# Performance work log

Hardware: AMD Instinct MI355X
Metric: run time of the kernel (lower is better)

Reference implementation:

```python
import jax, jax.numpy as jnp
import numpy as np

N = 4096
IN_F = 256
F = 64      # out_features
H = 4       # heads
NEG_SLOPE = 0.2


def setup_inputs() -> dict:
    key = jax.random.key(0)
    k1, k2, k3, k4 = jax.random.split(key, 4)
    x = jax.random.normal(k1, (N, IN_F), dtype=jnp.float32)
    # symmetric random binary adjacency with self-loops (avoids empty softmax rows)
    adj = jax.random.bernoulli(k2, 0.5, (N, N)).astype(jnp.float32)
    adj = jnp.clip(adj + adj.T, 0.0, 1.0)
    adj = jnp.maximum(adj, jnp.eye(N, dtype=jnp.float32))
    W = jax.random.normal(k3, (IN_F, F * H), dtype=jnp.float32) * (1.0 / np.sqrt(IN_F))
    a = jax.random.normal(k4, (2 * F, 1), dtype=jnp.float32) * 0.1
    return {"x": x, "adj": adj, "W": W, "a": a}


def reference(x, adj, W, a):
    # h: [N, H, F]
    h = (x @ W).reshape(N, H, F)
    # e[i, j, h] = leakyrelu(a_l . h[i, h] + a_r . h[j, h])  -- avoids the O(N^2*H*2F) concat
    a_l = a[:F, 0]
    a_r = a[F:, 0]
    el = jnp.einsum('nhf,f->nh', h, a_l)  # [N, H]
    er = jnp.einsum('nhf,f->nh', h, a_r)  # [N, H]
    e = jax.nn.leaky_relu(el[:, None, :] + er[None, :, :], NEG_SLOPE)  # [N, N, H]
    e = jnp.where(adj[:, :, None] == 0, -jnp.inf, e)
    attention = jax.nn.softmax(e, axis=1)  # softmax over neighbors j
    h_prime = jnp.einsum('ijh,jhf->ihf', attention, h)  # [N, H, F]
    return h_prime.mean(axis=1)  # [N, F]  (heads > 1 -> mean over heads)
```

## Files before the change

### kernel.cpp

```cpp
#include <hip/hip_runtime.h>
#include <hip/hip_bf16.h>

#define NN 4096
#define LOG2E 1.44269504088896340736f

typedef __attribute__((ext_vector_type(8))) short s8v;
typedef __attribute__((ext_vector_type(4))) float f4v;

__device__ __forceinline__ unsigned fu(float x){ union{float f;unsigned u;}z; z.f=x; return z.u; }
__device__ __forceinline__ unsigned short f2bf_rne(float x){
  unsigned u = fu(x);
  u += 0x7fffu + ((u >> 16) & 1u);
  return (unsigned short)(u >> 16);
}
__device__ __forceinline__ unsigned pack2_rne(float a, float b){
  return (unsigned)f2bf_rne(a) | ((unsigned)f2bf_rne(b) << 16);
}

__global__ __launch_bounds__(256) void k1_proj(
    const float* __restrict__ x, const float* __restrict__ W,
    const float* __restrict__ a, unsigned short* __restrict__ Vf,
    float* __restrict__ el4, float* __restrict__ Qr, float* __restrict__ Sr)
{
  __shared__ float4 xs[512];
  const int t = threadIdx.x;
  const int r0 = blockIdx.x * 8;
  const float4* xg = (const float4*)(x + (size_t)r0 * 256);
  xs[t] = xg[t];
  xs[t + 256] = xg[t + 256];
  __syncthreads();

  float acc[8] = {0.f,0.f,0.f,0.f,0.f,0.f,0.f,0.f};
  const float* Wp = W + t;
  float w0 = Wp[0], w1 = Wp[256], w2 = Wp[512], w3 = Wp[768];
  #pragma unroll 1
  for (int k4 = 0; k4 < 64; ++k4) {
    const int kn = (k4 + 1) & 63;
    float nw0 = Wp[kn*1024 +   0];
    float nw1 = Wp[kn*1024 + 256];
    float nw2 = Wp[kn*1024 + 512];
    float nw3 = Wp[kn*1024 + 768];
    #pragma unroll
    for (int r = 0; r < 8; ++r) {
      float4 xv = xs[r*64 + k4];
      acc[r] = fmaf(xv.x, w0, acc[r]);
      acc[r] = fmaf(xv.y, w1, acc[r]);
      acc[r] = fmaf(xv.z, w2, acc[r]);
      acc[r] = fmaf(xv.w, w3, acc[r]);
    }
    w0 = nw0; w1 = nw1; w2 = nw2; w3 = nw3;
  }

  union { unsigned u[4]; s8v v; } pk;
  #pragma unroll
  for (int p = 0; p < 4; ++p)
    pk.u[p] = pack2_rne(acc[2*p], acc[2*p+1]);
  {
    const int hh = t >> 6, nf = (t >> 4) & 3, mm = t & 15;
    const int jblk = r0 >> 5, qq = (r0 >> 3) & 3;
    const size_t chunk = (size_t)(((hh * 128 + jblk) * 4 + nf) * 64 + qq * 16 + mm);
    *(s8v*)(Vf + chunk * 8) = pk.v;
  }

  const int f = t & 63, h = t >> 6;
  const float al = a[f], ar = a[64 + f];
  #pragma unroll
  for (int r = 0; r < 8; ++r) {
    float v = acc[r] * al;
    float u = acc[r] * ar;
    #pragma unroll
    for (int off = 32; off > 0; off >>= 1) {
      v += __shfl_xor(v, off);
      u += __shfl_xor(u, off);
    }
    if (f == 0) {
      el4[(r0 + r) * 4 + h] = v * LOG2E;
      float up = u * LOG2E;
      Qr[h * NN + (r0 + r)] = __builtin_amdgcn_exp2f(up);
      Sr[h * NN + (r0 + r)] = __builtin_amdgcn_exp2f(0.2f * up);
    }
  }
}

__global__ __launch_bounds__(256, 8) void k0_pack(
    const float* __restrict__ adj, const float* __restrict__ el4,
    const float* __restrict__ Qr, const float* __restrict__ Sr,
    unsigned long long* __restrict__ adjB, float* __restrict__ lsum)
{
  __shared__ float qsh[2048];
  const int t = threadIdx.x;
  const int w = t >> 6, l = t & 63;
  const int p = blockIdx.y;
  const int row = blockIdx.x * 4 + w;
  const int jwin = p * 256;

  {
    const int h = t >> 6;
    float4 qv = *(const float4*)(Qr + h * NN + jwin + l * 4);
    float4 sv = *(const float4*)(Sr + h * NN + jwin + l * 4);
    *(float4*)(qsh + h * 256 + l * 4) = qv;
    *(float4*)(qsh + 1024 + h * 256 + l * 4) = sv;
  }

  const float4 av = *(const float4*)(adj + (size_t)row * NN + jwin + l * 4);

  unsigned long long b0 = __ballot(av.x != 0.0f);
  unsigned long long b1 = __ballot(av.y != 0.0f);
  unsigned long long b2 = __ballot(av.z != 0.0f);
  unsigned long long b3 = __ballot(av.w != 0.0f);
  if (l == 0) {
    unsigned long long* dst = adjB + (size_t)row * 64 + p * 4;
    dst[0] = b0; dst[1] = b1; dst[2] = b2; dst[3] = b3;
  }

  float4 elv = *(const float4*)(el4 + row * 4);
  const float P[4] = { __builtin_amdgcn_exp2f(elv.x), __builtin_amdgcn_exp2f(elv.y),
                       __builtin_amdgcn_exp2f(elv.z), __builtin_amdgcn_exp2f(elv.w) };
  const float R[4] = { __builtin_amdgcn_exp2f(0.2f*elv.x), __builtin_amdgcn_exp2f(0.2f*elv.y),
                       __builtin_amdgcn_exp2f(0.2f*elv.z), __builtin_amdgcn_exp2f(0.2f*elv.w) };

  __syncthreads();

  float ls[4];
  #pragma unroll
  for (int h = 0; h < 4; ++h) {
    float4 qv = *(const float4*)(qsh + h * 256 + l * 4);
    float4 sv = *(const float4*)(qsh + 1024 + h * 256 + l * 4);
    float s;
    s  = av.x * fmaxf(P[h] * qv.x, R[h] * sv.x);
    s  = fmaf(av.y, fmaxf(P[h] * qv.y, R[h] * sv.y), s);
    s  = fmaf(av.z, fmaxf(P[h] * qv.z, R[h] * sv.z), s);
    s  = fmaf(av.w, fmaxf(P[h] * qv.w, R[h] * sv.w), s);
    ls[h] = s;
  }
  #pragma unroll
  for (int h = 0; h < 4; ++h) {
    float v = ls[h];
    #pragma unroll
    for (int off = 32; off > 0; off >>= 1) v += __shfl_xor(v, off);
    ls[h] = v;
  }
  if (l == 0) {
    #pragma unroll
    for (int h = 0; h < 4; ++h)
      atomicAdd(&lsum[row * 4 + h], ls[h]);
  }
}

__global__ __launch_bounds__(256, 4) void k2_attn(
    const unsigned long long* __restrict__ adjB, const unsigned short* __restrict__ Vf,
    const float* __restrict__ el4, const float* __restrict__ lsum,
    const float* __restrict__ Qr, const float* __restrict__ Sr,
    float* __restrict__ out)
{
  __shared__ float qs[8192];
  const int t = threadIdx.x;
  const int w = t >> 6, l = t & 63;
  const int m = l & 15, q = l >> 4;
  const int i0 = blockIdx.x * 16;
  const int sw = blockIdx.y * 4 + w;
  const int i = i0 + m;
  const int jwin = sw * 256;

  {
    const int jc = l >> 3, qq = (l >> 1) & 3, hp = (l & 1) * 4;
    #pragma unroll
    for (int h = 0; h < 4; ++h) {
      float4 qv = *(const float4*)(Qr + h * NN + jwin + l * 4);
      float4 sv = *(const float4*)(Sr + h * NN + jwin + l * 4);
      float* cell = qs + (((w * 4 + h) * 8 + jc) * 4 + qq) * 16;
      *(float4*)(cell + hp) = qv;
      *(float4*)(cell + 8 + hp) = sv;
    }
  }

  float4 elv = *(const float4*)(el4 + i * 4);
  float4 ls4 = *(const float4*)(lsum + i * 4);
  float Pl[4], Rl[4];
  {
    const float el_[4] = {elv.x, elv.y, elv.z, elv.w};
    const float lv_[4] = {ls4.x, ls4.y, ls4.z, ls4.w};
    #pragma unroll
    for (int h = 0; h < 4; ++h) {
      const float inv = 1.0f / lv_[h];
      Pl[h] = __builtin_amdgcn_exp2f(el_[h]) * inv;
      Rl[h] = __builtin_amdgcn_exp2f(0.2f * el_[h]) * inv;
    }
  }

  const unsigned long long* bp = adjB + (size_t)i * 64 + sw * 4;
  unsigned long long b0 = bp[0], b1 = bp[1], b2 = bp[2], b3 = bp[3];

  f4v acc[4];
  #pragma unroll
  for (int nf = 0; nf < 4; ++nf) acc[nf] = (f4v){0.f, 0.f, 0.f, 0.f};

  const s8v* vfp = (const s8v*)Vf;
  s8v Bc[4];
  #pragma unroll
  for (int nf = 0; nf < 4; ++nf)
    Bc[nf] = vfp[(size_t)((0 * 128 + sw * 8 + 0) * 4 + nf) * 64 + l];

  #pragma unroll 1
  for (int jc = 0; jc < 8; ++jc) {
    const unsigned sh = jc * 8 + q * 2;
    const unsigned t0 = (unsigned)(b0 >> sh) & 3u;
    const unsigned t1 = (unsigned)(b1 >> sh) & 3u;
    const unsigned t2 = (unsigned)(b2 >> sh) & 3u;
    const unsigned t3 = (unsigned)(b3 >> sh) & 3u;
    float bitf[8];
    bitf[0] = (float)(t0 & 1u); bitf[4] = (float)(t0 >> 1);
    bitf[1] = (float)(t1 & 1u); bitf[5] = (float)(t1 >> 1);
    bitf[2] = (float)(t2 & 1u); bitf[6] = (float)(t2 >> 1);
    bitf[3] = (float)(t3 & 1u); bitf[7] = (float)(t3 >> 1);

    #pragma unroll
    for (int h = 0; h < 4; ++h) {
      const int hn = (h < 3) ? h + 1 : 0;
      const int jcn = (h < 3) ? jc : jc + 1;
      s8v Bn[4];
      #pragma unroll
      for (int nf = 0; nf < 4; ++nf)
        Bn[nf] = vfp[(size_t)((hn * 128 + sw * 8 + jcn) * 4 + nf) * 64 + l];

      const float* cell = qs + (((w * 4 + h) * 8 + jc) * 4 + q) * 16;
      float4 q0  = *(const float4*)(cell);
      float4 q1  = *(const float4*)(cell + 4);
      float4 sv0 = *(const float4*)(cell + 8);
      float4 sv1 = *(const float4*)(cell + 12);
      const float Ph = Pl[h], Rh = Rl[h];
      float s0 = bitf[0] * fmaxf(Ph * q0.x, Rh * sv0.x);
      float s1 = bitf[1] * fmaxf(Ph * q0.y, Rh * sv0.y);
      float s2 = bitf[2] * fmaxf(Ph * q0.z, Rh * sv0.z);
      float s3 = bitf[3] * fmaxf(Ph * q0.w, Rh * sv0.w);
      float s4 = bitf[4] * fmaxf(Ph * q1.x, Rh * sv1.x);
      float s5 = bitf[5] * fmaxf(Ph * q1.y, Rh * sv1.y);
      float s6 = bitf[6] * fmaxf(Ph * q1.z, Rh * sv1.z);
      float s7 = bitf[7] * fmaxf(Ph * q1.w, Rh * sv1.w);
      union { unsigned u[4]; s8v v; } A;
      A.u[0] = pack2_rne(s0, s1);
      A.u[1] = pack2_rne(s2, s3);
      A.u[2] = pack2_rne(s4, s5);
      A.u[3] = pack2_rne(s6, s7);
      #pragma unroll
      for (int nf = 0; nf < 4; ++nf)
        acc[nf] = __builtin_amdgcn_mfma_f32_16x16x32_bf16(A.v, Bc[nf], acc[nf], 0, 0, 0);
      #pragma unroll
      for (int nf = 0; nf < 4; ++nf) Bc[nf] = Bn[nf];
    }
  }

  __syncthreads();
  if (w > 0) {
    float* dst = qs + ((w - 1) * 64 + l) * 20;
    #pragma unroll
    for (int nf = 0; nf < 4; ++nf)
      *(f4v*)(dst + nf * 4) = acc[nf];
  }
  __syncthreads();
  if (w == 0) {
    const float* src = qs + l * 20;
    #pragma unroll
    for (int nf = 0; nf < 4; ++nf) {
      f4v s = acc[nf];
      s += *(const f4v*)(src +    0 + nf * 4);
      s += *(const f4v*)(src + 1280 + nf * 4);
      s += *(const f4v*)(src + 2560 + nf * 4);
      #pragma unroll
      for (int r = 0; r < 4; ++r) {
        int row = i0 + q * 4 + r;
        int col = nf * 16 + m;
        atomicAdd(&out[row * 64 + col], 0.25f * s[r]);
      }
    }
  }
}

extern "C" void kernel_launch(void* const* d_in, const int* in_sizes, int n_in,
                              void* d_out, int out_size, void* d_ws, size_t ws_size,
                              hipStream_t stream) {
  const float* x   = (const float*)d_in[0];
  const float* adj = (const float*)d_in[1];
  const float* W   = (const float*)d_in[2];
  const float* a   = (const float*)d_in[3];
  float* out = (float*)d_out;

  char* ws = (char*)d_ws;
  unsigned short* Vf = (unsigned short*)ws;
  float* el4 = (float*)(ws + (2u << 20));
  float* Qr  = (float*)(ws + (2u << 20) + (64u << 10));
  float* Sr  = (float*)(ws + (2u << 20) + (128u << 10));
  float* lsum= (float*)(ws + (2u << 20) + (192u << 10));
  unsigned long long* adjB = (unsigned long long*)(ws + (2u << 20) + (256u << 10));

  hipMemsetAsync(out, 0, (size_t)out_size * sizeof(float), stream);
  hipMemsetAsync(lsum, 0, NN * 4 * sizeof(float), stream);
  k1_proj<<<512, 256, 0, stream>>>(x, W, a, Vf, el4, Qr, Sr);
  k0_pack<<<dim3(1024, 16), 256, 0, stream>>>(adj, el4, Qr, Sr, adjB, lsum);
  k2_attn<<<dim3(256, 4), 256, 0, stream>>>(adjB, Vf, el4, lsum, Qr, Sr, out);
}
```

Measured before the change: 170.0 us.

## Coarsen adjacency pack kernel, replace lsum atomics with partial sums, deepen W prefetch

k0_pack now handles 1024 columns per block instead of 256. It issues four adjacency float4 loads up front and stages four windows of Q/S into shared memory. The per-row softmax denominators are written as four non-atomic partial sums, which k2_attn adds together. This removes the lsum memset and the atomic traffic. k1_proj also prefetches W two iterations ahead, at the cost of more registers and a larger shared array in k0 (32KB), which lowers occupancy.

Result: faster. 159.6 us (-6.1%).

```diff
diff --git a/kernel.cpp b/kernel.cpp
--- a/kernel.cpp
+++ b/kernel.cpp
@@ -32,10 +32,11 @@
 
   float acc[8] = {0.f,0.f,0.f,0.f,0.f,0.f,0.f,0.f};
   const float* Wp = W + t;
-  float w0 = Wp[0], w1 = Wp[256], w2 = Wp[512], w3 = Wp[768];
+  float wa0 = Wp[0],    wa1 = Wp[256],  wa2 = Wp[512],  wa3 = Wp[768];
+  float wb0 = Wp[1024], wb1 = Wp[1280], wb2 = Wp[1536], wb3 = Wp[1792];
   #pragma unroll 1
   for (int k4 = 0; k4 < 64; ++k4) {
-    const int kn = (k4 + 1) & 63;
+    const int kn = (k4 + 2) & 63;
     float nw0 = Wp[kn*1024 +   0];
     float nw1 = Wp[kn*1024 + 256];
     float nw2 = Wp[kn*1024 + 512];
@@ -43,12 +44,13 @@
     #pragma unroll
     for (int r = 0; r < 8; ++r) {
       float4 xv = xs[r*64 + k4];
-      acc[r] = fmaf(xv.x, w0, acc[r]);
-      acc[r] = fmaf(xv.y, w1, acc[r]);
-      acc[r] = fmaf(xv.z, w2, acc[r]);
-      acc[r] = fmaf(xv.w, w3, acc[r]);
-    }
-    w0 = nw0; w1 = nw1; w2 = nw2; w3 = nw3;
+      acc[r] = fmaf(xv.x, wa0, acc[r]);
+      acc[r] = fmaf(xv.y, wa1, acc[r]);
+      acc[r] = fmaf(xv.z, wa2, acc[r]);
+      acc[r] = fmaf(xv.w, wa3, acc[r]);
+    }
+    wa0 = wb0; wa1 = wb1; wa2 = wb2; wa3 = wb3;
+    wb0 = nw0; wb1 = nw1; wb2 = nw2; wb3 = nw3;
   }
 
   union { unsigned u[4]; s8v v; } pk;
@@ -82,35 +84,49 @@
   }
 }
 
-__global__ __launch_bounds__(256, 8) void k0_pack(
+__global__ __launch_bounds__(256, 4) void k0_pack(
     const float* __restrict__ adj, const float* __restrict__ el4,
     const float* __restrict__ Qr, const float* __restrict__ Sr,
-    unsigned long long* __restrict__ adjB, float* __restrict__ lsum)
+    unsigned long long* __restrict__ adjB, float* __restrict__ lsumP)
 {
-  __shared__ float qsh[2048];
+  __shared__ float qsh[8192];
   const int t = threadIdx.x;
   const int w = t >> 6, l = t & 63;
-  const int p = blockIdx.y;
   const int row = blockIdx.x * 4 + w;
-  const int jwin = p * 256;
+  const int p4 = blockIdx.y;
+  const int jbase = p4 * 1024;
+
+  const float* arow = adj + (size_t)row * NN + jbase + l * 4;
+  float4 av0 = *(const float4*)(arow);
+  float4 av1 = *(const float4*)(arow + 256);
+  float4 av2 = *(const float4*)(arow + 512);
+  float4 av3 = *(const float4*)(arow + 768);
 
   {
     const int h = t >> 6;
-    float4 qv = *(const float4*)(Qr + h * NN + jwin + l * 4);
-    float4 sv = *(const float4*)(Sr + h * NN + jwin + l * 4);
-    *(float4*)(qsh + h * 256 + l * 4) = qv;
-    *(float4*)(qsh + 1024 + h * 256 + l * 4) = sv;
-  }
-
-  const float4 av = *(const float4*)(adj + (size_t)row * NN + jwin + l * 4);
-
-  unsigned long long b0 = __ballot(av.x != 0.0f);
-  unsigned long long b1 = __ballot(av.y != 0.0f);
-  unsigned long long b2 = __ballot(av.z != 0.0f);
-  unsigned long long b3 = __ballot(av.w != 0.0f);
-  if (l == 0) {
-    unsigned long long* dst = adjB + (size_t)row * 64 + p * 4;
-    dst[0] = b0; dst[1] = b1; dst[2] = b2; dst[3] = b3;
+    #pragma unroll
+    for (int k = 0; k < 4; ++k) {
+      float4 qv = *(const float4*)(Qr + h * NN + jbase + k * 256 + l * 4);
+      float4 sv = *(const float4*)(Sr + h * NN + jbase + k * 256 + l * 4);
+      *(float4*)(qsh + ((k * 2 + 0) * 4 + h) * 256 + l * 4) = qv;
+      *(float4*)(qsh + ((k * 2 + 1) * 4 + h) * 256 + l * 4) = sv;
+    }
+  }
+
+  {
+    unsigned long long* dst = adjB + (size_t)row * 64 + p4 * 16;
+    const float4 avs[4] = {av0, av1, av2, av3};
+    #pragma unroll
+    for (int k = 0; k < 4; ++k) {
+      unsigned long long b0 = __ballot(avs[k].x != 0.0f);
+      unsigned long long b1 = __ballot(avs[k].y != 0.0f);
+      unsigned long long b2 = __ballot(avs[k].z != 0.0f);
+      unsigned long long b3 = __ballot(avs[k].w != 0.0f);
+      if (l == 0) {
+        dst[k * 4 + 0] = b0; dst[k * 4 + 1] = b1;
+        dst[k * 4 + 2] = b2; dst[k * 4 + 3] = b3;
+      }
+    }
   }
 
   float4 elv = *(const float4*)(el4 + row * 4);
@@ -121,17 +137,24 @@
 
   __syncthreads();
 
-  float ls[4];
-  #pragma unroll
-  for (int h = 0; h < 4; ++h) {
-    float4 qv = *(const float4*)(qsh + h * 256 + l * 4);
-    float4 sv = *(const float4*)(qsh + 1024 + h * 256 + l * 4);
-    float s;
-    s  = av.x * fmaxf(P[h] * qv.x, R[h] * sv.x);
-    s  = fmaf(av.y, fmaxf(P[h] * qv.y, R[h] * sv.y), s);
-    s  = fmaf(av.z, fmaxf(P[h] * qv.z, R[h] * sv.z), s);
-    s  = fmaf(av.w, fmaxf(P[h] * qv.w, R[h] * sv.w), s);
-    ls[h] = s;
+  float ls[4] = {0.f, 0.f, 0.f, 0.f};
+  {
+    const float4 avs[4] = {av0, av1, av2, av3};
+    #pragma unroll
+    for (int k = 0; k < 4; ++k) {
+      const float4 av = avs[k];
+      #pragma unroll
+      for (int h = 0; h < 4; ++h) {
+        float4 qv = *(const float4*)(qsh + ((k * 2 + 0) * 4 + h) * 256 + l * 4);
+        float4 sv = *(const float4*)(qsh + ((k * 2 + 1) * 4 + h) * 256 + l * 4);
+        float s;
+        s = av.x * fmaxf(P[h] * qv.x, R[h] * sv.x);
+        s = fmaf(av.y, fmaxf(P[h] * qv.y, R[h] * sv.y), s);
+        s = fmaf(av.z, fmaxf(P[h] * qv.z, R[h] * sv.z), s);
+        s = fmaf(av.w, fmaxf(P[h] * qv.w, R[h] * sv.w), s);
+        ls[h] += s;
+      }
+    }
   }
   #pragma unroll
   for (int h = 0; h < 4; ++h) {
@@ -140,16 +163,13 @@
     for (int off = 32; off > 0; off >>= 1) v += __shfl_xor(v, off);
     ls[h] = v;
   }
-  if (l == 0) {
-    #pragma unroll
-    for (int h = 0; h < 4; ++h)
-      atomicAdd(&lsum[row * 4 + h], ls[h]);
-  }
+  if (l == 0)
+    *(float4*)(lsumP + ((size_t)p4 * NN + row) * 4) = make_float4(ls[0], ls[1], ls[2], ls[3]);
 }
 
 __global__ __launch_bounds__(256, 4) void k2_attn(
     const unsigned long long* __restrict__ adjB, const unsigned short* __restrict__ Vf,
-    const float* __restrict__ el4, const float* __restrict__ lsum,
+    const float* __restrict__ el4, const float* __restrict__ lsumP,
     const float* __restrict__ Qr, const float* __restrict__ Sr,
     float* __restrict__ out)
 {
@@ -175,11 +195,16 @@
   }
 
   float4 elv = *(const float4*)(el4 + i * 4);
-  float4 ls4 = *(const float4*)(lsum + i * 4);
+  float lx = 0.f, ly = 0.f, lz = 0.f, lw = 0.f;
+  #pragma unroll
+  for (int p = 0; p < 4; ++p) {
+    float4 v = *(const float4*)(lsumP + ((size_t)p * NN + i) * 4);
+    lx += v.x; ly += v.y; lz += v.z; lw += v.w;
+  }
   float Pl[4], Rl[4];
   {
     const float el_[4] = {elv.x, elv.y, elv.z, elv.w};
-    const float lv_[4] = {ls4.x, ls4.y, ls4.z, ls4.w};
+    const float lv_[4] = {lx, ly, lz, lw};
     #pragma unroll
     for (int h = 0; h < 4; ++h) {
       const float inv = 1.0f / lv_[h];
@@ -287,15 +312,14 @@
 
   char* ws = (char*)d_ws;
   unsigned short* Vf = (unsigned short*)ws;
-  float* el4 = (float*)(ws + (2u << 20));
-  float* Qr  = (float*)(ws + (2u << 20) + (64u << 10));
-  float* Sr  = (float*)(ws + (2u << 20) + (128u << 10));
-  float* lsum= (float*)(ws + (2u << 20) + (192u << 10));
-  unsigned long long* adjB = (unsigned long long*)(ws + (2u << 20) + (256u << 10));
+  float* el4   = (float*)(ws + (2u << 20));
+  float* Qr    = (float*)(ws + (2u << 20) + (64u << 10));
+  float* Sr    = (float*)(ws + (2u << 20) + (128u << 10));
+  float* lsumP = (float*)(ws + (2u << 20) + (192u << 10));
+  unsigned long long* adjB = (unsigned long long*)(ws + (2u << 20) + (448u << 10));
 
   hipMemsetAsync(out, 0, (size_t)out_size * sizeof(float), stream);
-  hipMemsetAsync(lsum, 0, NN * 4 * sizeof(float), stream);
   k1_proj<<<512, 256, 0, stream>>>(x, W, a, Vf, el4, Qr, Sr);
-  k0_pack<<<dim3(1024, 16), 256, 0, stream>>>(adj, el4, Qr, Sr, adjB, lsum);
-  k2_attn<<<dim3(256, 4), 256, 0, stream>>>(adjB, Vf, el4, lsum, Qr, Sr, out);
-}
+  k0_pack<<<dim3(1024, 4), 256, 0, stream>>>(adj, el4, Qr, Sr, adjB, lsumP);
+  k2_attn<<<dim3(256, 4), 256, 0, stream>>>(adjB, Vf, el4, lsumP, Qr, Sr, out);
+}
```
